# Performance work log

Hardware: AMD Instinct MI355X
Metric: run time of the kernel (lower is better)

Reference implementation:

```python
import jax, jax.numpy as jnp
import numpy as np
import math

B, S, D = 2, 2048, 1024
H, HKV, HD = 16, 4, 64
SF = 4
SD = HD // SF  # sparsity proj dim = 16
TEMP = 1.0
INIT_STD = 0.02


def rope(qk):
    # qk: [b, h, s, d]
    d = qk.shape[-1]
    theta = 1.0 / (10000.0 ** (jnp.arange(0, d, 2, dtype=jnp.float32) / d))  # [d/2]
    s = jnp.arange(qk.shape[2], dtype=jnp.float32)
    freqs = jnp.outer(s, theta)                     # [s, d/2]
    freqs = jnp.concatenate([freqs, freqs], -1)     # [s, d]
    qk1, qk2 = jnp.split(qk, 2, axis=-1)
    rot = jnp.concatenate([-qk2, qk1], -1)
    return qk * jnp.cos(freqs) + rot * jnp.sin(freqs)


def setup_inputs() -> dict:
    key = jax.random.key(0)
    ks = jax.random.split(key, 8)
    x = jax.random.normal(ks[0], (B, S, D), dtype=jnp.float32)
    Wq = jax.random.normal(ks[1], (D, D), dtype=jnp.float32) * INIT_STD
    Wk = jax.random.normal(ks[2], (HKV * HD, D), dtype=jnp.float32) * INIT_STD
    Wv = jax.random.normal(ks[3], (HKV * HD, D), dtype=jnp.float32) * INIT_STD
    Wo = jax.random.normal(ks[4], (D, D), dtype=jnp.float32) * INIT_STD
    bo = jnp.zeros((D,), dtype=jnp.float32)
    Ws = jax.random.normal(ks[5], (SD, HD), dtype=jnp.float32) * INIT_STD
    bs = jnp.zeros((SD,), dtype=jnp.float32)
    return {"x": x, "Wq": Wq, "Wk": Wk, "Wv": Wv, "Wo": Wo, "bo": bo, "Ws": Ws, "bs": bs}


def reference(x, Wq, Wk, Wv, Wo, bo, Ws, bs):
    b, s, _ = x.shape
    # projections (torch Linear: x @ W.T)
    q = (x @ Wq.T).reshape(b, s, H, HD).transpose(0, 2, 1, 3)     # [b,H,s,hd]
    k = (x @ Wk.T).reshape(b, s, HKV, HD).transpose(0, 2, 1, 3)   # [b,Hkv,s,hd]
    v = (x @ Wv.T).reshape(b, s, HKV, HD).transpose(0, 2, 1, 3)
    q = rope(q)
    k = rope(k)
    n_rep = H // HKV
    k = jnp.repeat(k, n_rep, axis=1)  # [b,H,s,hd]
    v = jnp.repeat(v, n_rep, axis=1)
    # low-rank sparsity gate
    q_sp = q @ Ws.T + bs              # [b,H,s,sd]
    k_sp = k @ Ws.T + bs
    sp_scores = jnp.einsum('bhid,bhjd->bhij', q_sp, k_sp) / math.sqrt(SD)
    gate = jax.nn.sigmoid(sp_scores / TEMP)
    attn = jnp.einsum('bhid,bhjd->bhij', q, k) / math.sqrt(HD)
    attn = attn * gate
    causal = jnp.triu(jnp.ones((s, s), dtype=bool), k=1)
    attn = jnp.where(causal, -jnp.inf, attn)
    w = jax.nn.softmax(attn, axis=-1)
    out = jnp.einsum('bhij,bhjd->bhid', w, v)               # [b,H,s,hd]
    out = out.transpose(0, 2, 1, 3).reshape(b, s, H * HD)   # [b,s,D]
    return out @ Wo.T + bo
```

## Files before the change

### kernel.cpp

```cpp
#include <hip/hip_runtime.h>
#include <math.h>

#define B_ 2
#define S_ 2048
#define D_ 1024
#define H_ 16
#define HKV_ 4
#define HD_ 64
#define SD_ 16

typedef __attribute__((ext_vector_type(8))) short bf16x8;
typedef __attribute__((ext_vector_type(4))) float f32x4;
typedef __attribute__((ext_vector_type(8))) unsigned short us8;
typedef __attribute__((ext_vector_type(4))) unsigned short us4;

#define LOG2E 1.4426950408889634f

__device__ __forceinline__ unsigned short f2bf(float f) {
  unsigned int u = __builtin_bit_cast(unsigned int, f);
  u += 0x7fffu + ((u >> 16) & 1u);
  return (unsigned short)(u >> 16);
}

__device__ __forceinline__ void gload16(const unsigned short* g, unsigned short* l) {
  __builtin_amdgcn_global_load_lds(
      (const __attribute__((address_space(1))) unsigned int*)g,
      (__attribute__((address_space(3))) unsigned int*)l, 16, 0, 0);
}

__global__ __launch_bounds__(256) void convert_bf16(
    const float* __restrict__ x, const float* __restrict__ wq,
    const float* __restrict__ wk, const float* __restrict__ wv,
    const float* __restrict__ wo, unsigned short* __restrict__ xb,
    unsigned short* __restrict__ wqkv, unsigned short* __restrict__ wob) {
  const int blk = blockIdx.x;
  const float* src;
  unsigned short* dst;
  int off;
  if (blk < 2048)      { src = x;  dst = xb;             off = blk * 2048; }
  else if (blk < 2560) { src = wq; dst = wqkv;           off = (blk - 2048) * 2048; }
  else if (blk < 2688) { src = wk; dst = wqkv + 1048576; off = (blk - 2560) * 2048; }
  else if (blk < 2816) { src = wv; dst = wqkv + 1310720; off = (blk - 2688) * 2048; }
  else                 { src = wo; dst = wob;            off = (blk - 2816) * 2048; }
  const int i = off + threadIdx.x * 8;
  float4 a = *(const float4*)(src + i);
  float4 b = *(const float4*)(src + i + 4);
  us8 o;
  o[0] = f2bf(a.x); o[1] = f2bf(a.y); o[2] = f2bf(a.z); o[3] = f2bf(a.w);
  o[4] = f2bf(b.x); o[5] = f2bf(b.y); o[6] = f2bf(b.z); o[7] = f2bf(b.w);
  *(us8*)(dst + i) = o;
}

__global__ __launch_bounds__(256) void gemm_bf16(
    const unsigned short* __restrict__ A, const unsigned short* __restrict__ Bm,
    const float* __restrict__ bias, float* __restrict__ C, int N) {
  __shared__ unsigned short As[64 * 64];
  __shared__ unsigned short Bs[128 * 64];
  const int tid = threadIdx.x;
  const int w = tid >> 6, lane = tid & 63;
  const int nm = lane & 15, quad = lane >> 4;
  const int m0 = blockIdx.y * 64, n0 = blockIdx.x * 128;
  const int wn = w * 32;

  f32x4 acc[4][2] = {};
  int arow[2], acol[2], brow[4], bcol[4];
#pragma unroll
  for (int it = 0; it < 2; ++it) {
    int s = it * 256 + tid;
    arow[it] = s >> 3;
    acol[it] = ((s & 7) ^ (arow[it] & 7)) * 8;
  }
#pragma unroll
  for (int it = 0; it < 4; ++it) {
    int s = it * 256 + tid;
    brow[it] = s >> 3;
    bcol[it] = ((s & 7) ^ (brow[it] & 7)) * 8;
  }

  for (int k0 = 0; k0 < 1024; k0 += 64) {
    __syncthreads();
#pragma unroll
    for (int it = 0; it < 2; ++it)
      gload16(A + (size_t)(m0 + arow[it]) * 1024 + k0 + acol[it],
              &As[(it * 256 + w * 64) * 8]);
#pragma unroll
    for (int it = 0; it < 4; ++it)
      gload16(Bm + (size_t)(n0 + brow[it]) * 1024 + k0 + bcol[it],
              &Bs[(it * 256 + w * 64) * 8]);
    __syncthreads();

#pragma unroll
    for (int ks = 0; ks < 2; ++ks) {
      const int cq = ks * 4 + quad;
      bf16x8 af[4], bfr[2];
#pragma unroll
      for (int mi = 0; mi < 4; ++mi) {
        const int m = mi * 16 + nm;
        af[mi] = *(const bf16x8*)&As[(m * 8 + (cq ^ (m & 7))) * 8];
      }
#pragma unroll
      for (int ni = 0; ni < 2; ++ni) {
        const int n = wn + ni * 16 + nm;
        bfr[ni] = *(const bf16x8*)&Bs[(n * 8 + (cq ^ (n & 7))) * 8];
      }
#pragma unroll
      for (int mi = 0; mi < 4; ++mi)
#pragma unroll
        for (int ni = 0; ni < 2; ++ni)
          acc[mi][ni] = __builtin_amdgcn_mfma_f32_16x16x32_bf16(
              af[mi], bfr[ni], acc[mi][ni], 0, 0, 0);
    }
  }

  float bv[2] = {0.f, 0.f};
  if (bias) {
#pragma unroll
    for (int ni = 0; ni < 2; ++ni) bv[ni] = bias[n0 + wn + ni * 16 + nm];
  }
#pragma unroll
  for (int mi = 0; mi < 4; ++mi) {
#pragma unroll
    for (int r = 0; r < 4; ++r) {
      const int row = m0 + mi * 16 + quad * 4 + r;
      float* crow = C + (size_t)row * N + n0 + wn + nm;
#pragma unroll
      for (int ni = 0; ni < 2; ++ni) crow[ni * 16] = acc[mi][ni][r] + bv[ni];
    }
  }
}

__global__ __launch_bounds__(256) void rope_scatter(
    const float* __restrict__ P, const float* __restrict__ Ws,
    const float* __restrict__ bs, unsigned short* __restrict__ qh,
    unsigned short* __restrict__ kh, unsigned short* __restrict__ qsp,
    unsigned short* __restrict__ ksp) {
  __shared__ float wsl[16 * 64];
  __shared__ float bsl[16];
  __shared__ float rbuf[4][64];
  const int tid = threadIdx.x;
  const int row = blockIdx.x;
  const int b = row >> 11;
  const int s = row & 2047;
  {
    *(float4*)&wsl[tid * 4] = *(const float4*)&Ws[tid * 4];
    if (tid < 16) bsl[tid] = bs[tid];
  }
  __syncthreads();
  const int w = tid >> 6, lane = tid & 63;
  const int i = lane & 31, halfu = lane >> 5;
  const float theta = powf(10000.f, -((float)(2 * i) * (1.f / 64.f)));
  const float f = (float)s * theta;
  const float cf = cosf(f);
  const float sf = sinf(f);
  for (int slot = w; slot < 20; slot += 4) {
    float val = P[(size_t)row * 1536 + slot * 64 + lane];
    float partner = __shfl_xor(val, 32);
    float rot = halfu ? partner : -partner;
    float r = val * cf + rot * sf;
    unsigned short* dst;
    unsigned short* spdst;
    float qscale, spscale;
    if (slot < 16) {
      dst = qh + ((size_t)(b * 16 + slot) * 2048 + s) * 64;
      spdst = qsp + ((size_t)(b * 16 + slot) * 2048 + s) * 16;
      qscale = 0.125f * LOG2E; spscale = 0.25f * LOG2E;
    } else {
      int hh = slot - 16;
      dst = kh + ((size_t)(b * 4 + hh) * 2048 + s) * 64;
      spdst = ksp + ((size_t)(b * 4 + hh) * 2048 + s) * 16;
      qscale = 1.f; spscale = 1.f;
    }
    dst[lane] = f2bf(r * qscale);
    rbuf[w][lane] = r;
    int p = lane >> 4, j = lane & 15;
    float partial = 0.f;
#pragma unroll
    for (int t = 0; t < 16; ++t)
      partial += wsl[j * 64 + p * 16 + t] * rbuf[w][p * 16 + t];
    partial += __shfl_xor(partial, 16);
    partial += __shfl_xor(partial, 32);
    if (p == 0) spdst[j] = f2bf((partial + bsl[j]) * spscale);
  }
}

__global__ __launch_bounds__(256) void v_transpose(
    const float* __restrict__ proj, unsigned short* __restrict__ vt) {
  __shared__ unsigned short t_[64 * 72];
  const int bkv = blockIdx.y;
  const int s0 = blockIdx.x * 64;
  const int b = bkv >> 2, hkv = bkv & 3;
  const int tid = threadIdx.x;
  const int sl = tid >> 2;
  const int c0 = (tid & 3) * 16;
  const float* src = proj + ((size_t)b * 2048 + s0 + sl) * 1536 + 1280 + hkv * 64 + c0;
  us8 o0, o1;
#pragma unroll
  for (int t = 0; t < 8; ++t) { o0[t] = f2bf(src[t]); o1[t] = f2bf(src[8 + t]); }
  *(us8*)&t_[sl * 72 + c0] = o0;
  *(us8*)&t_[sl * 72 + c0 + 8] = o1;
  __syncthreads();
  const int d = tid >> 2;
  const int sc_ = (tid & 3) * 16;
  us8 w0, w1;
#pragma unroll
  for (int t = 0; t < 8; ++t) w0[t] = t_[(sc_ + t) * 72 + d];
#pragma unroll
  for (int t = 0; t < 8; ++t) w1[t] = t_[(sc_ + 8 + t) * 72 + d];
  unsigned short* dst = vt + (size_t)bkv * 131072 + (size_t)d * 2048 + s0 + sc_;
  *(us8*)dst = w0;
  *(us8*)(dst + 8) = w1;
}

__device__ __forceinline__ void attn_tile(
    const unsigned short* __restrict__ Ksb, const unsigned short* __restrict__ Vsb,
    const unsigned short* __restrict__ Kspb_, unsigned short* __restrict__ pw,
    bf16x8 qa0, bf16x8 qa1, bf16x8 qspa, int j0, int qrow0, int nm, int quad,
    float l_r[4], f32x4 O[4]) {
#pragma unroll
  for (int st = 0; st < 4; ++st) {
    if (j0 + st * 16 > qrow0 + 15) {
#pragma unroll
      for (int r = 0; r < 4; ++r) {
        const int prow = quad * 4 + r;
        const int chunk = (st * 2 + (nm >> 3)) ^ (prow & 7);
        pw[(prow * 8 + chunk) * 8 + (nm & 7)] = 0;
      }
      continue;
    }
    const int krow = st * 16 + nm;
    const int r7 = krow & 7;
    bf16x8 kb0 = *(const bf16x8*)&Ksb[(krow * 8 + (quad ^ r7)) * 8];
    bf16x8 kb1 = *(const bf16x8*)&Ksb[(krow * 8 + ((4 + quad) ^ r7)) * 8];
    bf16x8 gb = *(const bf16x8*)&Kspb_[(krow * 2 + (quad & 1)) * 8];
    f32x4 z = {0.f, 0.f, 0.f, 0.f};
    f32x4 s = __builtin_amdgcn_mfma_f32_16x16x32_bf16(qa0, kb0, z, 0, 0, 0);
    s = __builtin_amdgcn_mfma_f32_16x16x32_bf16(qa1, kb1, s, 0, 0, 0);
    f32x4 g = __builtin_amdgcn_mfma_f32_16x16x32_bf16(qspa, gb, z, 0, 0, 0);
    const bool edge = (j0 + st * 16 + 15 > qrow0);
#pragma unroll
    for (int r = 0; r < 4; ++r) {
      float gate = __builtin_amdgcn_rcpf(1.f + __builtin_amdgcn_exp2f(-g[r]));
      float v = s[r] * gate;
      if (edge) {
        const int col = j0 + st * 16 + nm;
        const int rowg = qrow0 + quad * 4 + r;
        v = (col > rowg) ? -INFINITY : v;
      }
      float p = __builtin_amdgcn_exp2f(v);
      l_r[r] += p;
      const int prow = quad * 4 + r;
      const int chunk = (st * 2 + (nm >> 3)) ^ (prow & 7);
      pw[(prow * 8 + chunk) * 8 + (nm & 7)] = f2bf(p);
    }
  }

#pragma unroll
  for (int c = 0; c < 2; ++c) {
    const int gc = c * 4 + quad;
    bf16x8 pa = *(const bf16x8*)&pw[(nm * 8 + (gc ^ (nm & 7))) * 8];
#pragma unroll
    for (int dt = 0; dt < 4; ++dt) {
      const int vrow = dt * 16 + nm;
      bf16x8 vb = *(const bf16x8*)&Vsb[(vrow * 8 + (gc ^ (vrow & 7))) * 8];
      O[dt] = __builtin_amdgcn_mfma_f32_16x16x32_bf16(pa, vb, O[dt], 0, 0, 0);
    }
  }
}

__global__ __launch_bounds__(256) void attn_kernel(
    const unsigned short* __restrict__ qh, const unsigned short* __restrict__ kh,
    const unsigned short* __restrict__ vt, const unsigned short* __restrict__ qsp,
    const unsigned short* __restrict__ ksp, unsigned short* __restrict__ ao) {
  __shared__ unsigned short Ks[2][64 * 64];
  __shared__ unsigned short Vs[2][64 * 64];
  __shared__ unsigned short Ksp[2][64 * 16];
  __shared__ unsigned short Pw[4][16 * 64];

  const int tid = threadIdx.x;
  const int w = tid >> 6;
  const int lane = tid & 63;
  const int nm = lane & 15;
  const int quad = lane >> 4;
  const int bh = blockIdx.y;
  const int b = bh >> 4, h = bh & 15;
  const int hkv = h >> 2;
  const size_t kbase = (size_t)(b * 4 + hkv) * 2048 * 64;
  const size_t vbase = (size_t)(b * 4 + hkv) * 131072;
  const size_t kspb = (size_t)(b * 4 + hkv) * 2048 * 16;

  int srow_[2], scol_[2];
#pragma unroll
  for (int rd = 0; rd < 2; ++rd) {
    int Lc = rd * 256 + w * 64 + lane;
    int r = Lc >> 3;
    srow_[rd] = r;
    scol_[rd] = ((Lc & 7) ^ (r & 7)) * 8;
  }
  unsigned short* pw = &Pw[w][0];

#define STAGE(BUF, J0)                                                         \
  {                                                                            \
    _Pragma("unroll")                                                          \
    for (int rd = 0; rd < 2; ++rd) {                                           \
      gload16(kh + kbase + (size_t)((J0) + srow_[rd]) * 64 + scol_[rd],        \
              &Ks[BUF][(rd * 256 + w * 64) * 8]);                              \
      gload16(vt + vbase + (size_t)srow_[rd] * 2048 + (J0) + scol_[rd],        \
              &Vs[BUF][(rd * 256 + w * 64) * 8]);                              \
    }                                                                          \
    if (w < 2) {                                                               \
      const int Lc = w * 64 + lane;                                            \
      gload16(ksp + kspb + (size_t)((J0) + (Lc >> 1)) * 16 + (Lc & 1) * 8,     \
              &Ksp[BUF][w * 512]);                                             \
    }                                                                          \
  }

  const int qxA = 31 - blockIdx.x;
  const int qxB = blockIdx.x;
  const int qrow0A = qxA * 64 + w * 16;
  const int qrow0B = qxB * 64 + w * 16;

  const size_t qbA = ((size_t)(b * 16 + h) * 2048 + qrow0A + nm) * 64;
  bf16x8 qa0A = *(const bf16x8*)(qh + qbA + quad * 8);
  bf16x8 qa1A = *(const bf16x8*)(qh + qbA + 32 + quad * 8);
  const size_t qbB = ((size_t)(b * 16 + h) * 2048 + qrow0B + nm) * 64;
  bf16x8 qa0B = *(const bf16x8*)(qh + qbB + quad * 8);
  bf16x8 qa1B = *(const bf16x8*)(qh + qbB + 32 + quad * 8);
  bf16x8 qspaA = {0, 0, 0, 0, 0, 0, 0, 0};
  bf16x8 qspaB = {0, 0, 0, 0, 0, 0, 0, 0};
  if (quad < 2) {
    qspaA = *(const bf16x8*)(qsp + ((size_t)(b * 16 + h) * 2048 + qrow0A + nm) * 16 + quad * 8);
    qspaB = *(const bf16x8*)(qsp + ((size_t)(b * 16 + h) * 2048 + qrow0B + nm) * 16 + quad * 8);
  }

  float l_r[4] = {0.f, 0.f, 0.f, 0.f};
  f32x4 O[4] = {{0.f, 0.f, 0.f, 0.f}, {0.f, 0.f, 0.f, 0.f},
                {0.f, 0.f, 0.f, 0.f}, {0.f, 0.f, 0.f, 0.f}};

  STAGE(0, 0);
  int cur = 0;
  for (int jt = 0; jt <= qxA; ++jt) {
    __syncthreads();
    if (jt < qxA) STAGE(cur ^ 1, (jt + 1) * 64)
    else          STAGE(cur ^ 1, 0)
    attn_tile(&Ks[cur][0], &Vs[cur][0], &Ksp[cur][0], pw,
              qa0A, qa1A, qspaA, jt * 64, qrow0A, nm, quad, l_r, O);
    cur ^= 1;
  }

#pragma unroll
  for (int r = 0; r < 4; ++r) {
    float v = l_r[r];
    v += __shfl_xor(v, 1);
    v += __shfl_xor(v, 2);
    v += __shfl_xor(v, 4);
    v += __shfl_xor(v, 8);
    const float inv = __builtin_amdgcn_rcpf(v);
    const int rowg = qrow0A + quad * 4 + r;
    unsigned short* orow = ao + ((size_t)b * 2048 + rowg) * 1024 + h * 64 + nm;
#pragma unroll
    for (int dt = 0; dt < 4; ++dt) orow[dt * 16] = f2bf(O[dt][r] * inv);
  }
#pragma unroll
  for (int dt = 0; dt < 4; ++dt) O[dt] = (f32x4){0.f, 0.f, 0.f, 0.f};
#pragma unroll
  for (int r = 0; r < 4; ++r) l_r[r] = 0.f;

  for (int jt = 0; jt <= qxB; ++jt) {
    __syncthreads();
    if (jt < qxB) STAGE(cur ^ 1, (jt + 1) * 64)
    attn_tile(&Ks[cur][0], &Vs[cur][0], &Ksp[cur][0], pw,
              qa0B, qa1B, qspaB, jt * 64, qrow0B, nm, quad, l_r, O);
    cur ^= 1;
  }

#pragma unroll
  for (int r = 0; r < 4; ++r) {
    float v = l_r[r];
    v += __shfl_xor(v, 1);
    v += __shfl_xor(v, 2);
    v += __shfl_xor(v, 4);
    v += __shfl_xor(v, 8);
    const float inv = __builtin_amdgcn_rcpf(v);
    const int rowg = qrow0B + quad * 4 + r;
    unsigned short* orow = ao + ((size_t)b * 2048 + rowg) * 1024 + h * 64 + nm;
#pragma unroll
    for (int dt = 0; dt < 4; ++dt) orow[dt * 16] = f2bf(O[dt][r] * inv);
  }
#undef STAGE
}

extern "C" void kernel_launch(void* const* d_in, const int* in_sizes, int n_in,
                              void* d_out, int out_size, void* d_ws,
                              size_t ws_size, hipStream_t stream) {
  const float* x = (const float*)d_in[0];
  const float* Wq = (const float*)d_in[1];
  const float* Wk = (const float*)d_in[2];
  const float* Wv = (const float*)d_in[3];
  const float* Wo = (const float*)d_in[4];
  const float* bo = (const float*)d_in[5];
  const float* Ws = (const float*)d_in[6];
  const float* bs = (const float*)d_in[7];
  float* out = (float*)d_out;

  char* wsb = (char*)d_ws;
  float* proj = (float*)wsb;
  unsigned short* aob  = (unsigned short*)wsb;
  unsigned short* qh   = (unsigned short*)(wsb + 25165824);
  unsigned short* kh   = (unsigned short*)(wsb + 33554432);
  unsigned short* vtb  = (unsigned short*)(wsb + 35651584);
  unsigned short* qsp  = (unsigned short*)(wsb + 37748736);
  unsigned short* ksp  = (unsigned short*)(wsb + 39845888);
  unsigned short* xb   = (unsigned short*)(wsb + 40370176);
  unsigned short* wqkv = (unsigned short*)(wsb + 48758784);
  unsigned short* wob  = (unsigned short*)(wsb + 51904512);

  convert_bf16<<<dim3(3328), 256, 0, stream>>>(x, Wq, Wk, Wv, Wo, xb, wqkv, wob);
  gemm_bf16<<<dim3(12, 64), 256, 0, stream>>>(xb, wqkv, nullptr, proj, 1536);
  rope_scatter<<<dim3(4096), 256, 0, stream>>>(proj, Ws, bs, qh, kh, qsp, ksp);
  v_transpose<<<dim3(32, 8), 256, 0, stream>>>(proj, vtb);
  attn_kernel<<<dim3(16, 32), 256, 0, stream>>>(qh, kh, vtb, qsp, ksp, aob);
  gemm_bf16<<<dim3(8, 64), 256, 0, stream>>>(aob, wob, bo, out, 1024);
}
```

Measured before the change: 207.1 us.

## Split key tile across two wave groups with shared-memory partial reduction

The attention block grows from 4 to 8 waves. Each pair of waves shares the same 16 query rows but handles half of the 64-key tile. Partial O and row sums are merged through shared memory before normalisation. The aim is to raise the number of waves per CU and hide the latency of the serial per-tile work. The cost is extra LDS for Ox/Lx, an extra barrier per query block, and no scaling of MFMA work per wave.

```diff
diff --git a/kernel.cpp b/kernel.cpp
--- a/kernel.cpp
+++ b/kernel.cpp
@@ -215,15 +215,16 @@
     const unsigned short* __restrict__ Ksb, const unsigned short* __restrict__ Vsb,
     const unsigned short* __restrict__ Kspb_, unsigned short* __restrict__ pw,
     bf16x8 qa0, bf16x8 qa1, bf16x8 qspa, int j0, int qrow0, int nm, int quad,
-    float l_r[4], f32x4 O[4]) {
-#pragma unroll
-  for (int st = 0; st < 4; ++st) {
+    int ws, float l_r[4], f32x4 O[4]) {
+#pragma unroll
+  for (int stl = 0; stl < 2; ++stl) {
+    const int st = ws * 2 + stl;
     if (j0 + st * 16 > qrow0 + 15) {
 #pragma unroll
       for (int r = 0; r < 4; ++r) {
         const int prow = quad * 4 + r;
-        const int chunk = (st * 2 + (nm >> 3)) ^ (prow & 7);
-        pw[(prow * 8 + chunk) * 8 + (nm & 7)] = 0;
+        const int chunk = (stl * 2 + (nm >> 3)) ^ (prow & 3);
+        pw[(prow * 4 + chunk) * 8 + (nm & 7)] = 0;
       }
       continue;
     }
@@ -249,35 +250,35 @@
       float p = __builtin_amdgcn_exp2f(v);
       l_r[r] += p;
       const int prow = quad * 4 + r;
-      const int chunk = (st * 2 + (nm >> 3)) ^ (prow & 7);
-      pw[(prow * 8 + chunk) * 8 + (nm & 7)] = f2bf(p);
-    }
-  }
-
-#pragma unroll
-  for (int c = 0; c < 2; ++c) {
-    const int gc = c * 4 + quad;
-    bf16x8 pa = *(const bf16x8*)&pw[(nm * 8 + (gc ^ (nm & 7))) * 8];
-#pragma unroll
-    for (int dt = 0; dt < 4; ++dt) {
-      const int vrow = dt * 16 + nm;
-      bf16x8 vb = *(const bf16x8*)&Vsb[(vrow * 8 + (gc ^ (vrow & 7))) * 8];
-      O[dt] = __builtin_amdgcn_mfma_f32_16x16x32_bf16(pa, vb, O[dt], 0, 0, 0);
-    }
-  }
-}
-
-__global__ __launch_bounds__(256) void attn_kernel(
+      const int chunk = (stl * 2 + (nm >> 3)) ^ (prow & 3);
+      pw[(prow * 4 + chunk) * 8 + (nm & 7)] = f2bf(p);
+    }
+  }
+
+  bf16x8 pa = *(const bf16x8*)&pw[(nm * 4 + (quad ^ (nm & 3))) * 8];
+#pragma unroll
+  for (int dt = 0; dt < 4; ++dt) {
+    const int vrow = dt * 16 + nm;
+    bf16x8 vb = *(const bf16x8*)&Vsb[(vrow * 8 + ((ws * 4 + quad) ^ (vrow & 7))) * 8];
+    O[dt] = __builtin_amdgcn_mfma_f32_16x16x32_bf16(pa, vb, O[dt], 0, 0, 0);
+  }
+}
+
+__global__ __launch_bounds__(512) void attn_kernel(
     const unsigned short* __restrict__ qh, const unsigned short* __restrict__ kh,
     const unsigned short* __restrict__ vt, const unsigned short* __restrict__ qsp,
     const unsigned short* __restrict__ ksp, unsigned short* __restrict__ ao) {
   __shared__ unsigned short Ks[2][64 * 64];
   __shared__ unsigned short Vs[2][64 * 64];
   __shared__ unsigned short Ksp[2][64 * 16];
-  __shared__ unsigned short Pw[4][16 * 64];
+  __shared__ unsigned short Pw[8][16 * 32];
+  __shared__ float Ox[4][16][64];
+  __shared__ float Lx[4][4][64];
 
   const int tid = threadIdx.x;
   const int w = tid >> 6;
+  const int ws = w >> 2;
+  const int wr = w & 3;
   const int lane = tid & 63;
   const int nm = lane & 15;
   const int quad = lane >> 4;
@@ -288,27 +289,18 @@
   const size_t vbase = (size_t)(b * 4 + hkv) * 131072;
   const size_t kspb = (size_t)(b * 4 + hkv) * 2048 * 16;
 
-  int srow_[2], scol_[2];
-#pragma unroll
-  for (int rd = 0; rd < 2; ++rd) {
-    int Lc = rd * 256 + w * 64 + lane;
-    int r = Lc >> 3;
-    srow_[rd] = r;
-    scol_[rd] = ((Lc & 7) ^ (r & 7)) * 8;
-  }
+  const int Lc = tid;
+  const int sr = Lc >> 3;
+  const int sc = ((Lc & 7) ^ (sr & 7)) * 8;
   unsigned short* pw = &Pw[w][0];
 
 #define STAGE(BUF, J0)                                                         \
   {                                                                            \
-    _Pragma("unroll")                                                          \
-    for (int rd = 0; rd < 2; ++rd) {                                           \
-      gload16(kh + kbase + (size_t)((J0) + srow_[rd]) * 64 + scol_[rd],        \
-              &Ks[BUF][(rd * 256 + w * 64) * 8]);                              \
-      gload16(vt + vbase + (size_t)srow_[rd] * 2048 + (J0) + scol_[rd],        \
-              &Vs[BUF][(rd * 256 + w * 64) * 8]);                              \
-    }                                                                          \
+    gload16(kh + kbase + (size_t)((J0) + sr) * 64 + sc,                        \
+            &Ks[BUF][(w * 64) * 8]);                                           \
+    gload16(vt + vbase + (size_t)sr * 2048 + (J0) + sc,                        \
+            &Vs[BUF][(w * 64) * 8]);                                           \
     if (w < 2) {                                                               \
-      const int Lc = w * 64 + lane;                                            \
       gload16(ksp + kspb + (size_t)((J0) + (Lc >> 1)) * 16 + (Lc & 1) * 8,     \
               &Ksp[BUF][w * 512]);                                             \
     }                                                                          \
@@ -316,8 +308,8 @@
 
   const int qxA = 31 - blockIdx.x;
   const int qxB = blockIdx.x;
-  const int qrow0A = qxA * 64 + w * 16;
-  const int qrow0B = qxB * 64 + w * 16;
+  const int qrow0A = qxA * 64 + wr * 16;
+  const int qrow0B = qxB * 64 + wr * 16;
 
   const size_t qbA = ((size_t)(b * 16 + h) * 2048 + qrow0A + nm) * 64;
   bf16x8 qa0A = *(const bf16x8*)(qh + qbA + quad * 8);
@@ -343,22 +335,34 @@
     if (jt < qxA) STAGE(cur ^ 1, (jt + 1) * 64)
     else          STAGE(cur ^ 1, 0)
     attn_tile(&Ks[cur][0], &Vs[cur][0], &Ksp[cur][0], pw,
-              qa0A, qa1A, qspaA, jt * 64, qrow0A, nm, quad, l_r, O);
+              qa0A, qa1A, qspaA, jt * 64, qrow0A, nm, quad, ws, l_r, O);
     cur ^= 1;
   }
 
-#pragma unroll
-  for (int r = 0; r < 4; ++r) {
-    float v = l_r[r];
-    v += __shfl_xor(v, 1);
-    v += __shfl_xor(v, 2);
-    v += __shfl_xor(v, 4);
-    v += __shfl_xor(v, 8);
-    const float inv = __builtin_amdgcn_rcpf(v);
-    const int rowg = qrow0A + quad * 4 + r;
-    unsigned short* orow = ao + ((size_t)b * 2048 + rowg) * 1024 + h * 64 + nm;
-#pragma unroll
-    for (int dt = 0; dt < 4; ++dt) orow[dt * 16] = f2bf(O[dt][r] * inv);
+  if (ws == 1) {
+#pragma unroll
+    for (int dt = 0; dt < 4; ++dt)
+#pragma unroll
+      for (int r = 0; r < 4; ++r) Ox[wr][dt * 4 + r][lane] = O[dt][r];
+#pragma unroll
+    for (int r = 0; r < 4; ++r) Lx[wr][r][lane] = l_r[r];
+  }
+  __syncthreads();
+  if (ws == 0) {
+#pragma unroll
+    for (int r = 0; r < 4; ++r) {
+      float v = l_r[r] + Lx[wr][r][lane];
+      v += __shfl_xor(v, 1);
+      v += __shfl_xor(v, 2);
+      v += __shfl_xor(v, 4);
+      v += __shfl_xor(v, 8);
+      const float inv = __builtin_amdgcn_rcpf(v);
+      const int rowg = qrow0A + quad * 4 + r;
+      unsigned short* orow = ao + ((size_t)b * 2048 + rowg) * 1024 + h * 64 + nm;
+#pragma unroll
+      for (int dt = 0; dt < 4; ++dt)
+        orow[dt * 16] = f2bf((O[dt][r] + Ox[wr][dt * 4 + r][lane]) * inv);
+    }
   }
 #pragma unroll
   for (int dt = 0; dt < 4; ++dt) O[dt] = (f32x4){0.f, 0.f, 0.f, 0.f};
@@ -369,22 +373,34 @@
     __syncthreads();
     if (jt < qxB) STAGE(cur ^ 1, (jt + 1) * 64)
     attn_tile(&Ks[cur][0], &Vs[cur][0], &Ksp[cur][0], pw,
-              qa0B, qa1B, qspaB, jt * 64, qrow0B, nm, quad, l_r, O);
+              qa0B, qa1B, qspaB, jt * 64, qrow0B, nm, quad, ws, l_r, O);
     cur ^= 1;
   }
 
-#pragma unroll
-  for (int r = 0; r < 4; ++r) {
-    float v = l_r[r];
-    v += __shfl_xor(v, 1);
-    v += __shfl_xor(v, 2);
-    v += __shfl_xor(v, 4);
-    v += __shfl_xor(v, 8);
-    const float inv = __builtin_amdgcn_rcpf(v);
-    const int rowg = qrow0B + quad * 4 + r;
-    unsigned short* orow = ao + ((size_t)b * 2048 + rowg) * 1024 + h * 64 + nm;
-#pragma unroll
-    for (int dt = 0; dt < 4; ++dt) orow[dt * 16] = f2bf(O[dt][r] * inv);
+  if (ws == 1) {
+#pragma unroll
+    for (int dt = 0; dt < 4; ++dt)
+#pragma unroll
+      for (int r = 0; r < 4; ++r) Ox[wr][dt * 4 + r][lane] = O[dt][r];
+#pragma unroll
+    for (int r = 0; r < 4; ++r) Lx[wr][r][lane] = l_r[r];
+  }
+  __syncthreads();
+  if (ws == 0) {
+#pragma unroll
+    for (int r = 0; r < 4; ++r) {
+      float v = l_r[r] + Lx[wr][r][lane];
+      v += __shfl_xor(v, 1);
+      v += __shfl_xor(v, 2);
+      v += __shfl_xor(v, 4);
+      v += __shfl_xor(v, 8);
+      const float inv = __builtin_amdgcn_rcpf(v);
+      const int rowg = qrow0B + quad * 4 + r;
+      unsigned short* orow = ao + ((size_t)b * 2048 + rowg) * 1024 + h * 64 + nm;
+#pragma unroll
+      for (int dt = 0; dt < 4; ++dt)
+        orow[dt * 16] = f2bf((O[dt][r] + Ox[wr][dt * 4 + r][lane]) * inv);
+    }
   }
 #undef STAGE
 }
@@ -418,6 +434,6 @@
   gemm_bf16<<<dim3(12, 64), 256, 0, stream>>>(xb, wqkv, nullptr, proj, 1536);
   rope_scatter<<<dim3(4096), 256, 0, stream>>>(proj, Ws, bs, qh, kh, qsp, ksp);
   v_transpose<<<dim3(32, 8), 256, 0, stream>>>(proj, vtb);
-  attn_kernel<<<dim3(16, 32), 256, 0, stream>>>(qh, kh, vtb, qsp, ksp, aob);
+  attn_kernel<<<dim3(16, 32), 512, 0, stream>>>(qh, kh, vtb, qsp, ksp, aob);
   gemm_bf16<<<dim3(8, 64), 256, 0, stream>>>(aob, wob, bo, out, 1024);
 }
```

Measured after the change: 194.4 us. 6.1% less time.
